# Kernel optimization log

Hardware: AMD Instinct MI355X
Metric: run time of the kernel (lower is better)

## Reference

```python
import jax, jax.numpy as jnp
import numpy as np

H = 256          # hidden_dim
E = 2 * H        # encoder output / attention embed dim = 512
MEL = 512        # mel_dim (must equal E for the original attention call to type-check)
NH = 8
HD = E // NH     # 64
B = 16
T = 128
V = 256          # vocab_size
NSPK = 100       # hardcoded speaker embedding rows
MAX_LEN = min(1000, T * 10)  # 1000 decode steps


def setup_inputs() -> dict:
    key = jax.random.key(0)
    ks = iter(jax.random.split(key, 40))

    def w(shape, s=0.05):
        return jax.random.normal(next(ks), shape, dtype=jnp.float32) * s

    return {
        'text_tokens': jax.random.randint(next(ks), (B, T), 0, V),
        'speaker_id': jax.random.randint(next(ks), (B,), 0, NSPK),
        'emb_text': w((V, H)),
        'emb_speaker': w((NSPK, H)),
        # bidirectional encoder LSTM (PyTorch gate order i,f,g,o)
        'enc_f_Wih': w((4 * H, H)), 'enc_f_Whh': w((4 * H, H)),
        'enc_f_bih': w((4 * H,)), 'enc_f_bhh': w((4 * H,)),
        'enc_b_Wih': w((4 * H, H)), 'enc_b_Whh': w((4 * H, H)),
        'enc_b_bih': w((4 * H,)), 'enc_b_bhh': w((4 * H,)),
        # multihead attention in/out projections
        'Wq': w((E, E)), 'bq': w((E,)),
        'Wk': w((E, E)), 'bk': w((E,)),
        'Wv': w((E, E)), 'bv': w((E,)),
        'Wo': w((E, E)), 'bo': w((E,)),
        # decoder LSTM (input dim = E + MEL); hidden state is re-zeroed every
        # step in the original (output state discarded), so Whh never acts.
        'dec_Wih': w((4 * H, E + MEL)), 'dec_Whh': w((4 * H, H)),
        'dec_bih': w((4 * H,)), 'dec_bhh': w((4 * H,)),
        'Wmel': w((MEL, H)), 'bmel': w((MEL,)),
        'Wstop': w((1, H)), 'bstop': w((1,)),
    }


def _lstm(x, Wih, Whh, bih, bhh, reverse=False):
    # x: [B, T, D] -> hidden sequence [B, T, H]
    Bx = x.shape[0]
    Hh = Whh.shape[1]
    h0 = jnp.zeros((Bx, Hh), x.dtype)

    def step(carry, xt):
        h, c = carry
        gates = xt @ Wih.T + bih + h @ Whh.T + bhh
        i, f, g, o = jnp.split(gates, 4, axis=-1)
        c = jax.nn.sigmoid(f) * c + jax.nn.sigmoid(i) * jnp.tanh(g)
        h = jax.nn.sigmoid(o) * jnp.tanh(c)
        return (h, c), h

    _, hs = jax.lax.scan(step, (h0, h0), jnp.swapaxes(x, 0, 1), reverse=reverse)
    return jnp.swapaxes(hs, 0, 1)


def reference(text_tokens, speaker_id, emb_text, emb_speaker,
              enc_f_Wih, enc_f_Whh, enc_f_bih, enc_f_bhh,
              enc_b_Wih, enc_b_Whh, enc_b_bih, enc_b_bhh,
              Wq, bq, Wk, bk, Wv, bv, Wo, bo,
              dec_Wih, dec_Whh, dec_bih, dec_bhh,
              Wmel, bmel, Wstop, bstop):
    # text + speaker embedding
    x = emb_text[text_tokens] + emb_speaker[speaker_id][:, None, :]   # [B,T,H]
    # bidirectional LSTM encoder
    enc_f = _lstm(x, enc_f_Wih, enc_f_Whh, enc_f_bih, enc_f_bhh)
    enc_b = _lstm(x, enc_b_Wih, enc_b_Whh, enc_b_bih, enc_b_bhh, reverse=True)
    enc = jnp.concatenate([enc_f, enc_b], axis=-1)                    # [B,T,E]

    # K/V projections are constant across decode steps -> hoist out of the loop
    K = (enc @ Wk.T + bk).reshape(B, T, NH, HD).transpose(0, 2, 1, 3)   # [B,NH,T,HD]
    Vv = (enc @ Wv.T + bv).reshape(B, T, NH, HD).transpose(0, 2, 1, 3)  # [B,NH,T,HD]
    scale = 1.0 / np.sqrt(HD).astype(np.float32)

    def step(mel_in, _):
        # single-query multihead attention (query = previous mel frame)
        q = (mel_in @ Wq.T + bq).reshape(B, NH, HD)                     # [B,NH,HD]
        w = jax.nn.softmax(jnp.einsum('bhd,bhtd->bht', q, K) * scale, axis=-1)
        ctx = jnp.einsum('bht,bhtd->bhd', w, Vv).reshape(B, E)
        attended = ctx @ Wo.T + bo                                      # [B,E]
        xin = jnp.concatenate([attended, mel_in], axis=-1)              # [B,E+MEL]
        # decoder LSTM single step from ZERO state each step (state discarded
        # in the original), so Whh term vanishes
        gates = xin @ dec_Wih.T + dec_bih + dec_bhh
        i, f, g, o = jnp.split(gates, 4, axis=-1)
        c = jax.nn.sigmoid(i) * jnp.tanh(g)
        h = jax.nn.sigmoid(o) * jnp.tanh(c)                             # [B,H]
        mel = h @ Wmel.T + bmel                                         # [B,MEL]
        stop = h @ Wstop.T + bstop                                      # [B,1]
        return mel, (mel, stop, w.mean(axis=1))

    mel0 = jnp.zeros((B, MEL), jnp.float32)
    _, (mels, stops, attns) = jax.lax.scan(step, mel0, None, length=MAX_LEN)

    mel_output = jnp.swapaxes(mels, 0, 1)    # [B,MAX_LEN,MEL]
    stop_output = jnp.swapaxes(stops, 0, 1)  # [B,MAX_LEN,1]
    attn_last = attns[-1][:, None, :]        # [B,1,T] (head-averaged, last step)
    return mel_output, stop_output, attn_last
```

## Files before the change

kernel.cpp:

```cpp
#include <hip/hip_runtime.h>
#include <hip/hip_bf16.h>


typedef unsigned short u16;
typedef unsigned int   u32;
#define DI __device__ __forceinline__

static constexpr size_t WS_BAR   = 0;
static constexpr size_t WS_GBUF  = 64*1024;
static constexpr size_t WS_HBUF  = 192*1024;
static constexpr size_t WS_PROBS = 208*1024;
static constexpr size_t WS_BIAS  = 272*1024;
static constexpr size_t WS_W2M   = 320*1024;
static constexpr size_t WS_WQH   = 832*1024;
static constexpr size_t WS_WCG   = 1344*1024;

static constexpr size_t OF_ENC_A = 262144;
static constexpr size_t OF_ENC_B = 1286144;
static constexpr size_t OF_XWF   = 4015744;
static constexpr size_t OF_XWB   = 6112896;

DI float bf2f(u16 u){ union{u32 i; float f;} v; v.i = ((u32)u)<<16; return v.f; }
DI u16 f2bf(float f){ union{float f; u32 i;} v; v.f = f;
  u32 r = v.i + 0x7fffu + ((v.i>>16)&1u); return (u16)(r>>16); }
DI float2 bf2x(u32 u){ union{u32 i; float f;} a,b; a.i = u<<16; b.i = u & 0xffff0000u;
  float2 r; r.x = a.f; r.y = b.f; return r; }
DI float dot8(uint4 wv, float4 a, float4 b){
  float2 w0 = bf2x(wv.x), w1 = bf2x(wv.y), w2 = bf2x(wv.z), w3 = bf2x(wv.w);
  return w0.x*a.x + w0.y*a.y + w1.x*a.z + w1.y*a.w
       + w2.x*b.x + w2.y*b.y + w3.x*b.z + w3.y*b.w;
}
DI float dot8f(float4 wa, float4 wb, float4 a, float4 b){
  return wa.x*a.x + wa.y*a.y + wa.z*a.z + wa.w*a.w
       + wb.x*b.x + wb.y*b.y + wb.z*b.z + wb.w*b.w;
}
DI float sigm(float x){ return 1.f/(1.f + __expf(-x)); }

DI float afload(const float* p){
  return __hip_atomic_load(p, __ATOMIC_RELAXED, __HIP_MEMORY_SCOPE_AGENT);
}
DI void afstore(float* p, float v){
  __hip_atomic_store(p, v, __ATOMIC_RELAXED, __HIP_MEMORY_SCOPE_AGENT);
}
DI void aadd(float* p, float v){
  __hip_atomic_fetch_add(p, v, __ATOMIC_RELAXED, __HIP_MEMORY_SCOPE_AGENT);
}

DI void bar_arrive(int* flags, int myidx, int t){
  __syncthreads();
  if (threadIdx.x == 0){
    __builtin_amdgcn_s_waitcnt(0);
    __hip_atomic_store(flags + myidx*32, t, __ATOMIC_RELAXED, __HIP_MEMORY_SCOPE_AGENT);
  }
}
DI void bar_wait(int* flags, int n, int t){
  if (threadIdx.x < 64){
    const int idx = threadIdx.x & (n-1);
    int v = __hip_atomic_load(flags + idx*32, __ATOMIC_RELAXED, __HIP_MEMORY_SCOPE_AGENT);
    while (__any(v < t)){
      __builtin_amdgcn_s_sleep(1);
      if (v < t)
        v = __hip_atomic_load(flags + idx*32, __ATOMIC_RELAXED, __HIP_MEMORY_SCOPE_AGENT);
    }
  }
  __asm__ __volatile__("" ::: "memory");
  __syncthreads();
}

__global__ __launch_bounds__(256) void k_init(int* bars, float* hbuf){
  const int i = blockIdx.x*256 + threadIdx.x;
  for (int k = i; k < 49152; k += 32*256) bars[k] = 0;
  if (i < 4096) hbuf[i] = 0.f;
}

__global__ __launch_bounds__(256) void k_xw(
    const int* __restrict__ tok, const int* __restrict__ spk,
    const float* __restrict__ et, const float* __restrict__ es,
    const float* __restrict__ WihF, const float* __restrict__ bihF, const float* __restrict__ bhhF,
    const float* __restrict__ WihB, const float* __restrict__ bihB, const float* __restrict__ bhhB,
    float* __restrict__ xwf, float* __restrict__ xwb){
  const int tid = threadIdx.x, bi = blockIdx.x;
  const int dir = bi & 1, jc = (bi >> 1) & 3, btg = bi >> 3;
  const int j = jc*256 + tid;
  const float* W = (dir ? WihB : WihF) + j*256;
  const float bias = (dir ? bihB : bihF)[j] + (dir ? bhhB : bhhF)[j];
  float* xw = dir ? xwb : xwf;

  __shared__ __align__(16) float lx[8][256];
  #pragma unroll
  for (int r = 0; r < 8; ++r){
    const int bt = btg*8 + r;
    lx[r][tid] = et[tok[bt]*256 + tid] + es[spk[bt>>7]*256 + tid];
  }
  __syncthreads();

  float acc[8];
  #pragma unroll
  for (int k2 = 0; k2 < 8; ++k2) acc[k2] = bias;
  for (int h = 0; h < 256; h += 8){
    float4 w0 = *(const float4*)(W + h);
    float4 w1 = *(const float4*)(W + h + 4);
    #pragma unroll
    for (int k2 = 0; k2 < 8; ++k2)
      acc[k2] += dot8f(w0, w1, *(const float4*)(&lx[k2][h]), *(const float4*)(&lx[k2][h+4]));
  }
  #pragma unroll
  for (int k2 = 0; k2 < 8; ++k2) xw[(btg*8 + k2)*1024 + j] = acc[k2];
}

__global__ __launch_bounds__(256) void k_fuse(
    const float* __restrict__ decW, const float* __restrict__ Wo,
    const float* __restrict__ Wmel, const float* __restrict__ Wq,
    u16* __restrict__ Wcg, u16* __restrict__ W2m, float* __restrict__ Wqh){
  const int tid = threadIdx.x, blk = blockIdx.x;
  float acc[4] = {0.f,0.f,0.f,0.f};
  if (blk < 512){
    const int g0 = (blk >> 1)*4, e = (blk & 1)*256 + tid;
    for (int jj = 0; jj < 512; ++jj){
      float wo = Wo[jj*512 + e];
      #pragma unroll
      for (int i2 = 0; i2 < 4; ++i2) acc[i2] += decW[(g0+i2)*1024 + jj] * wo;
    }
    #pragma unroll
    for (int i2 = 0; i2 < 4; ++i2) Wcg[(g0+i2)*512 + e] = f2bf(acc[i2]);
  } else if (blk < 768){
    const int g0 = (blk - 512)*4, h = tid;
    for (int m = 0; m < 512; ++m){
      float wm = Wmel[m*256 + h];
      #pragma unroll
      for (int i2 = 0; i2 < 4; ++i2) acc[i2] += decW[(g0+i2)*1024 + 512 + m] * wm;
    }
    #pragma unroll
    for (int i2 = 0; i2 < 4; ++i2) W2m[(g0+i2)*256 + h] = f2bf(acc[i2]);
  } else {
    const int j0 = (blk - 768)*4, h = tid;
    for (int e = 0; e < 512; ++e){
      float wm = Wmel[e*256 + h];
      #pragma unroll
      for (int i2 = 0; i2 < 4; ++i2) acc[i2] += Wq[(j0+i2)*512 + e] * wm;
    }
    #pragma unroll
    for (int i2 = 0; i2 < 4; ++i2) Wqh[(j0+i2)*256 + h] = acc[i2];
  }
}

__global__ __launch_bounds__(256) void k_bias(
    const float* __restrict__ Wq, const float* __restrict__ bq, const float* __restrict__ bmel,
    const float* __restrict__ decW, const float* __restrict__ bo,
    const float* __restrict__ bih, const float* __restrict__ bhh, float* __restrict__ biasws){
  const int o = blockIdx.x*256 + threadIdx.x;
  if (o < 512){
    float s = bq[o];
    for (int e = 0; e < 512; ++e) s += Wq[o*512 + e] * bmel[e];
    biasws[o] = s;
  } else {
    const int gr = o - 512;
    float s1 = bih[gr] + bhh[gr];
    for (int jj = 0; jj < 512; ++jj) s1 += decW[gr*1024 + jj] * bo[jj];
    biasws[512 + gr] = s1;
    float s2 = s1;
    for (int m = 0; m < 512; ++m) s2 += decW[gr*1024 + 512 + m] * bmel[m];
    biasws[1536 + gr] = s2;
  }
}

__global__ __launch_bounds__(128) void k_enc(
    const float* __restrict__ xwf, const float* __restrict__ xwb,
    const float* __restrict__ WhhF, const float* __restrict__ WhhB,
    float* encA, float* encB, int* bars){
  const int tid = threadIdx.x;
  const int xcd = blockIdx.x & 7, sl = blockIdx.x >> 3;
  const int grp = xcd*4 + (sl >> 3);
  const int w = sl & 7;
  const int dir = grp & 1, b = grp >> 1;
  int* bar = bars + (16 + grp)*1024;
  const float* Whh = dir ? WhhB : WhhF;
  const float* xw = dir ? xwb : xwf;
  float* encb = (b < 8 ? encA : encB) + (size_t)(b & 7)*65536;
  const int q = tid >> 5, ii = tid & 31;
  const int j = q*256 + w*32 + ii;
  const float* wr = Whh + j*256;

  __shared__ __align__(16) float l_h[256];
  __shared__ float l_g[4][32];
  __shared__ float l_c[32];
  if (tid < 32) l_c[tid] = 0.f;
  __syncthreads();

  for (int it = 0; it < 128; ++it){
    const int ts = dir ? (127 - it) : it;
    float acc = xw[(b*128 + ts)*1024 + j];
    if (it > 0){
      const int tp = dir ? (ts + 1) : (ts - 1);
      const float* hp = encb + tp*512 + dir*256;
      for (int i = tid; i < 256; i += 128) l_h[i] = afload(hp + i);
      __syncthreads();
      #pragma unroll 4
      for (int k = 0; k < 256; k += 8)
        acc += dot8f(*(const float4*)(wr + k), *(const float4*)(wr + k + 4),
                     *(const float4*)(&l_h[k]), *(const float4*)(&l_h[k + 4]));
    }
    l_g[q][ii] = acc;
    __syncthreads();
    if (tid < 32){
      float ig = l_g[0][tid], fg = l_g[1][tid], gg = l_g[2][tid], og = l_g[3][tid];
      float c = sigm(fg)*l_c[tid] + sigm(ig)*tanhf(gg);
      l_c[tid] = c;
      afstore(encb + ts*512 + dir*256 + w*32 + tid, sigm(og)*tanhf(c));
    }
    bar_arrive(bar, w, it+1);
    bar_wait(bar, 8, it+1);
  }
}

__global__ __launch_bounds__(256) void k_proj(
    const float* __restrict__ encA, const float* __restrict__ encB,
    const float* __restrict__ Wk, const float* __restrict__ bk,
    const float* __restrict__ Wv, const float* __restrict__ bv,
    float* outf){
  const int tid = threadIdx.x, x = blockIdx.x;
  const int role = x & 1, dc = (x >> 1) & 1, btg = x >> 2;
  const int row = dc*256 + tid;
  const float* W = (role ? Wv : Wk) + row*512;
  const float bias = (role ? bv : bk)[row];
  const int b = (btg*8) >> 7;
  const float* eb = (b < 8 ? encA : encB) + (size_t)(b & 7)*65536;
  float acc[8];
  #pragma unroll
  for (int k2 = 0; k2 < 8; ++k2) acc[k2] = bias;
  for (int e = 0; e < 512; e += 8){
    float4 wa = *(const float4*)(W + e);
    float4 wb = *(const float4*)(W + e + 4);
    #pragma unroll
    for (int k2 = 0; k2 < 8; ++k2){
      const float* ep = eb + ((btg*8 + k2) & 127)*512 + e;
      acc[k2] += dot8f(wa, wb, *(const float4*)(ep), *(const float4*)(ep + 4));
    }
  }
  const int head = row >> 6, dd = row & 63;
  float* kv = outf + (size_t)(b >> 1)*1024000 + (size_t)(b & 1)*131072;
  #pragma unroll
  for (int k2 = 0; k2 < 8; ++k2){
    const int ts = (btg*8 + k2) & 127;
    if (role == 0) kv[head*8192 + ts*64 + dd] = acc[k2];
    else           kv[65536 + head*8192 + dd*128 + ts] = acc[k2];
  }
}

__global__ __launch_bounds__(512) void k_decode(
    const float* __restrict__ Wqh,
    const u16*   __restrict__ Wcg,
    const u16*   __restrict__ W2m,
    const float* __restrict__ Wmel,
    const float* __restrict__ bmel,
    const float* __restrict__ Wstop, const float* __restrict__ bstop,
    const float* __restrict__ bq,
    const float* __restrict__ biasws,
    float* Gbuf,
    float* probs, int* bars,
    float* out){
  const int tid = threadIdx.x;
  const int b = blockIdx.x & 15, sidx = blockIdx.x >> 4;
  const int h = sidx >> 1, half = sidx & 1;
  const int d = tid & 63, ko = tid >> 6;
  int* bflag = bars + b*512;
  float* out_mel  = out;
  float* out_stop = out + 8192000;
  float* out_attn = out + 8208000;

  __shared__ __align__(16) float lK[128*68];
  __shared__ __align__(16) float lV[64*132];
  __shared__ __align__(16) float l_h[256];
  __shared__ __align__(16) float l_hw[8*36];
  __shared__ __align__(16) float l_q[64];
  __shared__ __align__(16) float l_p[128];
  __shared__ __align__(16) float l_ct[64];
  __shared__ __align__(16) float l_qt[8][64];
  __shared__ __align__(16) float l_mt[8][64];
  __shared__ float l_sp[256];
  __shared__ float l_r[4];
  __shared__ float l_pad[1400];

  {
    const float* kv = out + (size_t)(b >> 1)*1024000 + (size_t)(b & 1)*131072;
    const float* gK = kv + h*8192;
    const float* gV = kv + 65536 + h*8192;
    for (int i = tid; i < 2048; i += 512){
      const int r = i >> 4, c = i & 15;
      *(float4*)(lK + r*68 + c*4) = *(const float4*)(gK + r*64 + c*4);
    }
    for (int i = tid; i < 2048; i += 512){
      const int r = i >> 5, c = i & 31;
      *(float4*)(lV + r*132 + c*4) = *(const float4*)(gV + r*128 + c*4);
    }
    if (tid < 32) l_pad[tid] = (float)tid;
  }

  float4 wq[8];
  {
    const float* p = Wqh + (h*64 + d)*256 + ko*32;
    #pragma unroll
    for (int j = 0; j < 8; ++j) wq[j] = *(const float4*)(p + 4*j);
  }
  const int rg = tid >> 2, c4 = tid & 3;
  uint4 wcg[3][2];
  #pragma unroll
  for (int s = 0; s < 3; ++s){
    const int r = half*384 + rg*3 + s;
    const int orig = r + (r >= 256 ? 256 : 0);
    const u16* p = Wcg + orig*512 + h*64 + c4*16;
    wcg[s][0] = *(const uint4*)(p);
    wcg[s][1] = *(const uint4*)(p + 8);
  }
  const int rw = tid >> 3, c8 = tid & 7;
  const int r2 = half*384 + h*48 + rw;
  uint4 w2[4];
  {
    const int orig2 = r2 + (r2 >= 256 ? 256 : 0);
    const u16* p = W2m + (tid < 384 ? orig2*256 + c8*32 : 0);
    #pragma unroll
    for (int j = 0; j < 4; ++j) w2[j] = *(const uint4*)(p + 8*j);
  }
  const float bq0 = bq[h*64 + d];
  const float bq1 = biasws[h*64 + d];
  const float bm  = bmel[h*64 + d];
  float bgi0=0, bgg0=0, bgo0=0, bgi1=0, bgg1=0, bgo1=0;
  if (tid < 256){
    bgi0 = biasws[ 512 + tid]; bgg0 = biasws[1024 + tid]; bgo0 = biasws[1280 + tid];
    bgi1 = biasws[1536 + tid]; bgg1 = biasws[2048 + tid]; bgo1 = biasws[2304 + tid];
  }
  const float wst = (tid < 256) ? Wstop[tid] : 0.f;
  const float bst = bstop[0];

  if (tid < 256) l_h[tid] = 0.f;
  if (tid < 288) l_hw[tid] = 0.f;
  float hreg = 0.f;
  __syncthreads();

  int rot = 0;
  for (int t = 0; t < 1000; ++t){
    float* buf = Gbuf + (rot*16 + b)*768;
    {
      const float4* hh = (const float4*)(l_h + ko*32);
      l_qt[ko][d] = dot8f(wq[0], wq[1], hh[0], hh[1]) + dot8f(wq[2], wq[3], hh[2], hh[3])
                  + dot8f(wq[4], wq[5], hh[4], hh[5]) + dot8f(wq[6], wq[7], hh[6], hh[7]);
    }
    if (tid < 384){
      const float4* hh = (const float4*)(l_hw + c8*36);
      float w2p = dot8(w2[0], hh[0], hh[1]) + dot8(w2[1], hh[2], hh[3])
                + dot8(w2[2], hh[4], hh[5]) + dot8(w2[3], hh[6], hh[7]);
      w2p += __shfl_xor(w2p, 1);
      w2p += __shfl_xor(w2p, 2);
      w2p += __shfl_xor(w2p, 4);
      if (c8 == 0) aadd(buf + r2, w2p);
    }
    __syncthreads();
    if (tid < 64){
      float qq = (t == 0 ? bq0 : bq1);
      #pragma unroll
      for (int k = 0; k < 8; ++k) qq += l_qt[k][tid];
      l_q[tid] = qq;
      __asm__ __volatile__("s_waitcnt lgkmcnt(0)" ::: "memory");
      const float* kr0 = lK + tid*68;
      const float* kr1 = lK + (tid + 64)*68;
      float s0 = 0.f, s1 = 0.f;
      #pragma unroll
      for (int k = 0; k < 64; k += 8){
        float4 qa = *(const float4*)(l_q + k), qb = *(const float4*)(l_q + k + 4);
        s0 += dot8f(*(const float4*)(kr0 + k), *(const float4*)(kr0 + k + 4), qa, qb);
        s1 += dot8f(*(const float4*)(kr1 + k), *(const float4*)(kr1 + k + 4), qa, qb);
      }
      s0 *= 0.125f; s1 *= 0.125f;
      float m = fmaxf(s0, s1);
      #pragma unroll
      for (int off = 32; off; off >>= 1) m = fmaxf(m, __shfl_xor(m, off));
      float p0 = __expf(s0 - m), p1 = __expf(s1 - m);
      float ss = p0 + p1;
      #pragma unroll
      for (int off = 32; off; off >>= 1) ss += __shfl_xor(ss, off);
      l_p[tid] = p0; l_p[tid + 64] = p1;
      if (tid == 0) l_r[0] = ss;
    }
    __syncthreads();
    {
      const float* vr = lV + d*132 + ko*16;
      const float* pp = l_p + ko*16;
      l_qt[ko][d] = dot8f(*(const float4*)(vr),     *(const float4*)(vr + 4),
                          *(const float4*)(pp),     *(const float4*)(pp + 4))
                  + dot8f(*(const float4*)(vr + 8), *(const float4*)(vr + 12),
                          *(const float4*)(pp + 8), *(const float4*)(pp + 12));
    }
    __syncthreads();
    if (tid < 64){
      float cs = 0.f;
      #pragma unroll
      for (int k = 0; k < 8; ++k) cs += l_qt[k][tid];
      l_ct[tid] = cs / l_r[0];
    }
    __syncthreads();
    {
      const float4* ct = (const float4*)(l_ct + c4*16);
      float pr0 = dot8(wcg[0][0], ct[0], ct[1]) + dot8(wcg[0][1], ct[2], ct[3]);
      float pr1 = dot8(wcg[1][0], ct[0], ct[1]) + dot8(wcg[1][1], ct[2], ct[3]);
      float pr2 = dot8(wcg[2][0], ct[0], ct[1]) + dot8(wcg[2][1], ct[2], ct[3]);
      pr0 += __shfl_xor(pr0, 1); pr0 += __shfl_xor(pr0, 2);
      pr1 += __shfl_xor(pr1, 1); pr1 += __shfl_xor(pr1, 2);
      pr2 += __shfl_xor(pr2, 1); pr2 += __shfl_xor(pr2, 2);
      if (c4 == 0){
        const int rb = half*384 + rg*3;
        aadd(buf + rb,     pr0);
        aadd(buf + rb + 1, pr1);
        aadd(buf + rb + 2, pr2);
      }
    }
    if (t >= 2 && tid < 48){
      int rr = rot + 1; if (rr == 3) rr = 0;
      afstore(Gbuf + (rr*16 + b)*768 + sidx*48 + tid, 0.f);
    }
    bar_arrive(bflag, sidx, t+1);
    if (t == 1) bar_wait(bars + (b ^ 1)*512, 16, 1);
    if (half == 0 && t > 0){
      const float* pm = Wmel + (h*64 + d)*256 + ko*32;
      const float4* hh = (const float4*)(l_h + ko*32);
      float4 a0 = *(const float4*)(pm);      float4 a1 = *(const float4*)(pm + 4);
      float4 a2 = *(const float4*)(pm + 8);  float4 a3 = *(const float4*)(pm + 12);
      float mp = dot8f(a0, a1, hh[0], hh[1]) + dot8f(a2, a3, hh[2], hh[3]);
      a0 = *(const float4*)(pm + 16); a1 = *(const float4*)(pm + 20);
      a2 = *(const float4*)(pm + 24); a3 = *(const float4*)(pm + 28);
      mp += dot8f(a0, a1, hh[4], hh[5]) + dot8f(a2, a3, hh[6], hh[7]);
      l_mt[ko][d] = mp;
    }
    if (h == 0 && half == 0 && t > 0 && tid < 256) l_sp[tid] = wst * hreg;
    __syncthreads();
    if (half == 0 && t > 0){
      if (tid < 64){
        float mv = bm;
        #pragma unroll
        for (int k = 0; k < 8; ++k) mv += l_mt[k][tid];
        out_mel[((size_t)b*1000 + (t-1))*512 + h*64 + tid] = mv;
      } else if (tid < 128 && h == 0){
        const int i4 = (tid & 63)*4;
        float sp = l_sp[i4] + l_sp[i4+1] + l_sp[i4+2] + l_sp[i4+3];
        #pragma unroll
        for (int off = 32; off; off >>= 1) sp += __shfl_xor(sp, off);
        if ((tid & 63) == 0) out_stop[b*1000 + (t-1)] = sp + bst;
      }
    }
    bar_wait(bflag, 16, t+1);
    if (tid < 256){
      float gi = (t == 0 ? bgi0 : bgi1) + afload(buf + tid);
      float gg = (t == 0 ? bgg0 : bgg1) + afload(buf + 256 + tid);
      float go = (t == 0 ? bgo0 : bgo1) + afload(buf + 512 + tid);
      float c = sigm(gi) * tanhf(gg);
      hreg = sigm(go) * tanhf(c);
      l_h[tid] = hreg;
      l_hw[(tid >> 5)*36 + (tid & 31)] = hreg;
    }
    __syncthreads();
    rot = (rot == 2) ? 0 : rot + 1;
  }

  if (half == 0){
    const float* pm = Wmel + (h*64 + d)*256 + ko*32;
    const float4* hh = (const float4*)(l_h + ko*32);
    float4 a0 = *(const float4*)(pm);      float4 a1 = *(const float4*)(pm + 4);
    float4 a2 = *(const float4*)(pm + 8);  float4 a3 = *(const float4*)(pm + 12);
    float mp = dot8f(a0, a1, hh[0], hh[1]) + dot8f(a2, a3, hh[2], hh[3]);
    a0 = *(const float4*)(pm + 16); a1 = *(const float4*)(pm + 20);
    a2 = *(const float4*)(pm + 24); a3 = *(const float4*)(pm + 28);
    mp += dot8f(a0, a1, hh[4], hh[5]) + dot8f(a2, a3, hh[6], hh[7]);
    l_mt[ko][d] = mp;
  }
  if (h == 0 && half == 0 && tid < 256) l_sp[tid] = wst * hreg;
  __syncthreads();
  if (half == 0){
    if (tid < 64){
      float mv = bm;
      #pragma unroll
      for (int k = 0; k < 8; ++k) mv += l_mt[k][tid];
      out_mel[((size_t)b*1000 + 999)*512 + h*64 + tid] = mv;
    } else if (tid >= 64 && tid < 128 && h == 0){
      const int i4 = (tid & 63)*4;
      float sp = l_sp[i4] + l_sp[i4+1] + l_sp[i4+2] + l_sp[i4+3];
      #pragma unroll
      for (int off = 32; off; off >>= 1) sp += __shfl_xor(sp, off);
      if ((tid & 63) == 0) out_stop[b*1000 + 999] = sp + bst;
    }
    if (tid < 128)
      afstore(probs + (b*8 + h)*128 + tid, l_p[tid] / l_r[0]);
  }
  bar_arrive(bflag, sidx, 1001);
  if (h == 0 && half == 0){
    bar_wait(bflag, 16, 1001);
    if (tid < 128){
      float ssum = 0.f;
      #pragma unroll
      for (int hh = 0; hh < 8; ++hh) ssum += afload(probs + (b*8 + hh)*128 + tid);
      out_attn[b*128 + tid] = ssum * 0.125f;
    }
  }
}

extern "C" void kernel_launch(void* const* d_in, const int* in_sizes, int n_in,
                              void* d_out, int out_size, void* d_ws, size_t ws_size,
                              hipStream_t stream){
  const int*   tok = (const int*)d_in[0];
  const int*   spk = (const int*)d_in[1];
  const float* emb_text = (const float*)d_in[2];
  const float* emb_spk  = (const float*)d_in[3];
  const float* WihF = (const float*)d_in[4];
  const float* WhhF = (const float*)d_in[5];
  const float* bihF = (const float*)d_in[6];
  const float* bhhF = (const float*)d_in[7];
  const float* WihB = (const float*)d_in[8];
  const float* WhhB = (const float*)d_in[9];
  const float* bihB = (const float*)d_in[10];
  const float* bhhB = (const float*)d_in[11];
  const float* Wq = (const float*)d_in[12];
  const float* bq = (const float*)d_in[13];
  const float* Wk = (const float*)d_in[14];
  const float* bk = (const float*)d_in[15];
  const float* Wv = (const float*)d_in[16];
  const float* bv = (const float*)d_in[17];
  const float* Wo = (const float*)d_in[18];
  const float* bo = (const float*)d_in[19];
  const float* decW = (const float*)d_in[20];
  const float* bih = (const float*)d_in[22];
  const float* bhh = (const float*)d_in[23];
  const float* Wmel = (const float*)d_in[24];
  const float* bmel = (const float*)d_in[25];
  const float* Wstop = (const float*)d_in[26];
  const float* bstop = (const float*)d_in[27];

  char* ws = (char*)d_ws;
  int*   bars   = (int*)(ws + WS_BAR);
  float* Gbuf   = (float*)(ws + WS_GBUF);
  float* hbuf   = (float*)(ws + WS_HBUF);
  float* probs  = (float*)(ws + WS_PROBS);
  float* biasws = (float*)(ws + WS_BIAS);
  u16*   W2m    = (u16*)(ws + WS_W2M);
  float* Wqh    = (float*)(ws + WS_WQH);
  u16*   Wcg    = (u16*)(ws + WS_WCG);

  float* outf = (float*)d_out;
  float* encA = outf + OF_ENC_A;
  float* encB = outf + OF_ENC_B;
  float* xwf  = outf + OF_XWF;
  float* xwb  = outf + OF_XWB;

  k_init <<<32,   256, 0, stream>>>(bars, hbuf);
  k_xw   <<<2048, 256, 0, stream>>>(tok, spk, emb_text, emb_spk,
                                    WihF, bihF, bhhF, WihB, bihB, bhhB, xwf, xwb);
  k_enc  <<<256,  128, 0, stream>>>(xwf, xwb, WhhF, WhhB, encA, encB, bars);
  k_fuse <<<896,  256, 0, stream>>>(decW, Wo, Wmel, Wq, Wcg, W2m, Wqh);
  k_bias <<<6,    256, 0, stream>>>(Wq, bq, bmel, decW, bo, bih, bhh, biasws);
  k_proj <<<1024, 256, 0, stream>>>(encA, encB, Wk, bk, Wv, bv, outf);
  k_decode<<<256, 512, 0, stream>>>(Wqh, Wcg, W2m, Wmel, bmel, Wstop, bstop,
                                    bq, biasws, Gbuf, probs, bars, outf);
}
```

Before: 6.618 ms.

## Precompute Wcg·V per head so decode step uses probabilities directly

Before the decode loop, each block multiplies its slice of the combined weight matrix by the per-head V tile, giving a 384x128 bf16 matrix held in LDS. Each step can then apply this matrix straight to the unnormalized attention probabilities, which drops the separate context reduction, two __syncthreads and the l_ct stage from the serial per-step path. Normalization becomes a multiply by a precomputed reciprocal. The cost is extra one-time setup work, a large LDS allocation that may lower occupancy, and bf16 rounding of the fused product.

```diff
diff --git a/kernel.cpp b/kernel.cpp
--- a/kernel.cpp
+++ b/kernel.cpp
@@ -269,31 +269,56 @@
   float* out_attn = out + 8208000;
 
   __shared__ __align__(16) float lK[128*68];
-  __shared__ __align__(16) float lV[64*132];
+  __shared__ __align__(16) u16  lWV[384*136];
   __shared__ __align__(16) float l_h[256];
   __shared__ __align__(16) float l_hw[8*36];
   __shared__ __align__(16) float l_q[64];
   __shared__ __align__(16) float l_p[128];
-  __shared__ __align__(16) float l_ct[64];
   __shared__ __align__(16) float l_qt[8][64];
   __shared__ __align__(16) float l_mt[8][64];
   __shared__ float l_sp[256];
   __shared__ float l_r[4];
-  __shared__ float l_pad[1400];
+
+  const float* kv = out + (size_t)(b >> 1)*1024000 + (size_t)(b & 1)*131072;
+  const int rg = tid >> 2, c4 = tid & 3;
+  const int rw = tid >> 3, c8 = tid & 7;
+  const int r2 = half*384 + h*48 + rw;
 
   {
-    const float* kv = out + (size_t)(b >> 1)*1024000 + (size_t)(b & 1)*131072;
+    const float* gV = kv + 65536 + h*8192;
+    for (int i = tid; i < 8192; i += 512){
+      const int dd = i >> 7, t = i & 127;
+      lK[t*68 + dd] = gV[i];
+    }
+  }
+  __syncthreads();
+  {
+    #pragma unroll
+    for (int s = 0; s < 3; ++s){
+      const int rpk = half*384 + rg*3 + s;
+      const int orig = rpk + (rpk >= 256 ? 256 : 0);
+      const u16* wp = Wcg + orig*512 + h*64;
+      uint4 w0 = *(const uint4*)(wp),      w1 = *(const uint4*)(wp + 8);
+      uint4 w2_ = *(const uint4*)(wp + 16), w3 = *(const uint4*)(wp + 24);
+      uint4 w4 = *(const uint4*)(wp + 32), w5 = *(const uint4*)(wp + 40);
+      uint4 w6 = *(const uint4*)(wp + 48), w7 = *(const uint4*)(wp + 56);
+      for (int t = c4*32; t < c4*32 + 32; ++t){
+        const float4* vv = (const float4*)(lK + t*68);
+        float acc = dot8(w0, vv[0], vv[1])  + dot8(w1, vv[2], vv[3])
+                  + dot8(w2_, vv[4], vv[5]) + dot8(w3, vv[6], vv[7])
+                  + dot8(w4, vv[8], vv[9])  + dot8(w5, vv[10], vv[11])
+                  + dot8(w6, vv[12], vv[13])+ dot8(w7, vv[14], vv[15]);
+        lWV[(rg*3 + s)*136 + t] = f2bf(acc);
+      }
+    }
+  }
+  __syncthreads();
+  {
     const float* gK = kv + h*8192;
-    const float* gV = kv + 65536 + h*8192;
     for (int i = tid; i < 2048; i += 512){
       const int r = i >> 4, c = i & 15;
       *(float4*)(lK + r*68 + c*4) = *(const float4*)(gK + r*64 + c*4);
     }
-    for (int i = tid; i < 2048; i += 512){
-      const int r = i >> 5, c = i & 31;
-      *(float4*)(lV + r*132 + c*4) = *(const float4*)(gV + r*128 + c*4);
-    }
-    if (tid < 32) l_pad[tid] = (float)tid;
   }
 
   float4 wq[8];
@@ -302,18 +327,6 @@
     #pragma unroll
     for (int j = 0; j < 8; ++j) wq[j] = *(const float4*)(p + 4*j);
   }
-  const int rg = tid >> 2, c4 = tid & 3;
-  uint4 wcg[3][2];
-  #pragma unroll
-  for (int s = 0; s < 3; ++s){
-    const int r = half*384 + rg*3 + s;
-    const int orig = r + (r >= 256 ? 256 : 0);
-    const u16* p = Wcg + orig*512 + h*64 + c4*16;
-    wcg[s][0] = *(const uint4*)(p);
-    wcg[s][1] = *(const uint4*)(p + 8);
-  }
-  const int rw = tid >> 3, c8 = tid & 7;
-  const int r2 = half*384 + h*48 + rw;
   uint4 w2[4];
   {
     const int orig2 = r2 + (r2 >= 256 ? 256 : 0);
@@ -379,38 +392,31 @@
       #pragma unroll
       for (int off = 32; off; off >>= 1) ss += __shfl_xor(ss, off);
       l_p[tid] = p0; l_p[tid + 64] = p1;
-      if (tid == 0) l_r[0] = ss;
+      if (tid == 0){ l_r[0] = ss; l_r[1] = 1.f/ss; }
     }
     __syncthreads();
     {
-      const float* vr = lV + d*132 + ko*16;
-      const float* pp = l_p + ko*16;
-      l_qt[ko][d] = dot8f(*(const float4*)(vr),     *(const float4*)(vr + 4),
-                          *(const float4*)(pp),     *(const float4*)(pp + 4))
-                  + dot8f(*(const float4*)(vr + 8), *(const float4*)(vr + 12),
-                          *(const float4*)(pp + 8), *(const float4*)(pp + 12));
-    }
-    __syncthreads();
-    if (tid < 64){
-      float cs = 0.f;
-      #pragma unroll
-      for (int k = 0; k < 8; ++k) cs += l_qt[k][tid];
-      l_ct[tid] = cs / l_r[0];
-    }
-    __syncthreads();
-    {
-      const float4* ct = (const float4*)(l_ct + c4*16);
-      float pr0 = dot8(wcg[0][0], ct[0], ct[1]) + dot8(wcg[0][1], ct[2], ct[3]);
-      float pr1 = dot8(wcg[1][0], ct[0], ct[1]) + dot8(wcg[1][1], ct[2], ct[3]);
-      float pr2 = dot8(wcg[2][0], ct[0], ct[1]) + dot8(wcg[2][1], ct[2], ct[3]);
-      pr0 += __shfl_xor(pr0, 1); pr0 += __shfl_xor(pr0, 2);
-      pr1 += __shfl_xor(pr1, 1); pr1 += __shfl_xor(pr1, 2);
-      pr2 += __shfl_xor(pr2, 1); pr2 += __shfl_xor(pr2, 2);
+      const float invS = l_r[1];
+      const float4* pp = (const float4*)(l_p + c4*32);
+      float4 pa0 = pp[0], pa1 = pp[1], pa2 = pp[2], pa3 = pp[3];
+      float4 pa4 = pp[4], pa5 = pp[5], pa6 = pp[6], pa7 = pp[7];
+      const u16* wr0 = lWV + (rg*3)*136 + c4*32;
+      float a0 = dot8(*(const uint4*)(wr0),      pa0, pa1) + dot8(*(const uint4*)(wr0 + 8),  pa2, pa3)
+               + dot8(*(const uint4*)(wr0 + 16), pa4, pa5) + dot8(*(const uint4*)(wr0 + 24), pa6, pa7);
+      const u16* wr1 = wr0 + 136;
+      float a1 = dot8(*(const uint4*)(wr1),      pa0, pa1) + dot8(*(const uint4*)(wr1 + 8),  pa2, pa3)
+               + dot8(*(const uint4*)(wr1 + 16), pa4, pa5) + dot8(*(const uint4*)(wr1 + 24), pa6, pa7);
+      const u16* wr2 = wr1 + 136;
+      float a2 = dot8(*(const uint4*)(wr2),      pa0, pa1) + dot8(*(const uint4*)(wr2 + 8),  pa2, pa3)
+               + dot8(*(const uint4*)(wr2 + 16), pa4, pa5) + dot8(*(const uint4*)(wr2 + 24), pa6, pa7);
+      a0 += __shfl_xor(a0, 1); a0 += __shfl_xor(a0, 2);
+      a1 += __shfl_xor(a1, 1); a1 += __shfl_xor(a1, 2);
+      a2 += __shfl_xor(a2, 1); a2 += __shfl_xor(a2, 2);
       if (c4 == 0){
         const int rb = half*384 + rg*3;
-        aadd(buf + rb,     pr0);
-        aadd(buf + rb + 1, pr1);
-        aadd(buf + rb + 2, pr2);
+        aadd(buf + rb,     a0*invS);
+        aadd(buf + rb + 1, a1*invS);
+        aadd(buf + rb + 2, a2*invS);
       }
     }
     if (t >= 2 && tid < 48){
```

New measurement: 6.871 ms. 3.8% more time.
